# Kernel tuning notes

Measured on AMD Instinct MI355X. Metric: run time of the kernel, lower is better.

## Reference

```python
import jax, jax.numpy as jnp
import numpy as np

N_NODES = 100000
N_EDGES = 3200000
IN_DIM = 256
UNITS = 128


def setup_inputs() -> dict:
    key = jax.random.key(0)
    k1, k2, k3, k4, k5 = jax.random.split(key, 5)
    x = jax.random.normal(k1, (N_NODES, IN_DIM), dtype=jnp.float32)
    kernel = jax.random.normal(k2, (IN_DIM, UNITS), dtype=jnp.float32) * (1.0 / np.sqrt(IN_DIM))
    adj_rows = jax.random.randint(k3, (N_EDGES,), 0, N_NODES, dtype=jnp.int32)
    adj_cols = jax.random.randint(k4, (N_EDGES,), 0, N_NODES, dtype=jnp.int32)
    adj_vals = jax.random.uniform(k5, (N_EDGES,), dtype=jnp.float32)
    return {"x": x, "kernel": kernel, "adj_rows": adj_rows,
            "adj_cols": adj_cols, "adj_vals": adj_vals}


def reference(x, kernel, adj_rows, adj_cols, adj_vals):
    # Dense transform: [N, in_dim] @ [in_dim, units] -> [N, units]
    h = jnp.matmul(x, kernel)
    # SpMM: out[r] = sum_{edges e with row r} val[e] * h[col[e]]
    msgs = h[adj_cols] * adj_vals[:, None]            # [E, units] gather
    agg = jax.ops.segment_sum(msgs, adj_rows, num_segments=N_NODES)  # scatter-add
    # use_bias=False -> no bias add. Activation: relu.
    return jax.nn.relu(agg)
```

## Files before the change

kernel.cpp:

```cpp
#include <hip/hip_runtime.h>
#include <hip/hip_fp16.h>

#define UNITS 128
#define IN_DIM 256

#define BSHIFT 6
#define BROWS  64
#define NBMAX  1600
#define BCAP   2368
#define SEDGE  2816
#define BIN_SLICE 4096

#define GR   128
#define GKC  64
#define APAD 36
#define BPAD 72

typedef short bf16x8 __attribute__((ext_vector_type(8)));
typedef float f32x4  __attribute__((ext_vector_type(4)));
union FragU { uint4 u; bf16x8 f; };

__device__ inline unsigned short bf16_bits(float a) {
  unsigned u = __float_as_uint(a);
  return (unsigned short)((u + 0x7FFF + ((u >> 16) & 1)) >> 16);
}
__device__ inline unsigned pack_bf16x2(float a, float b) {
  return (unsigned)bf16_bits(a) | ((unsigned)bf16_bits(b) << 16);
}

__global__ __launch_bounds__(256) void wt_kernel(
    const float* __restrict__ W, unsigned short* __restrict__ WT) {
  const int i = blockIdx.x * 256 + threadIdx.x;
  const int k = i >> 7;
  const int n = i & 127;
  WT[n * IN_DIM + k] = bf16_bits(W[i]);
}

__device__ __forceinline__ void do_bin(
    int* sh_cnt, int bid,
    const int* __restrict__ rows, const int* __restrict__ cols,
    const float* __restrict__ vals, int* __restrict__ bcount,
    int2* __restrict__ binned, int n_edges, int nbuckets) {
  const int tid = threadIdx.x;
  const int e0 = bid * BIN_SLICE;
  const int e_end = min(e0 + BIN_SLICE, n_edges);

  for (int i = tid; i < nbuckets; i += 512) sh_cnt[i] = 0;
  __syncthreads();
#pragma unroll
  for (int p = 0; p < 2; ++p) {
    const int e = e0 + (tid + p * 512) * 4;
    if (e < e_end) {
      const int4 r4 = *(const int4*)(rows + e);
      atomicAdd(&sh_cnt[r4.x >> BSHIFT], 1);
      atomicAdd(&sh_cnt[r4.y >> BSHIFT], 1);
      atomicAdd(&sh_cnt[r4.z >> BSHIFT], 1);
      atomicAdd(&sh_cnt[r4.w >> BSHIFT], 1);
    }
  }
  __syncthreads();
  for (int i = tid; i < nbuckets; i += 512) {
    const int c = sh_cnt[i];
    sh_cnt[i] = c ? atomicAdd(&bcount[i], c) : 0;
  }
  __syncthreads();
#pragma unroll
  for (int p = 0; p < 2; ++p) {
    const int e = e0 + (tid + p * 512) * 4;
    if (e < e_end) {
      const int4   r4 = *(const int4*)(rows + e);
      const int4   c4 = *(const int4*)(cols + e);
      const float4 v4 = *(const float4*)(vals + e);
#pragma unroll
      for (int u = 0; u < 4; ++u) {
        const int rr = (&r4.x)[u];
        const int cc = (&c4.x)[u];
        const int b  = rr >> BSHIFT;
        const int pos = atomicAdd(&sh_cnt[b], 1);
        if (pos < BCAP)
          binned[(size_t)b * BCAP + pos] = make_int2(
              (int)(((unsigned)(rr & (BROWS - 1)) << 25) | ((unsigned)cc << 8)),
              __float_as_int((&v4.x)[u]));
      }
    }
  }
  __syncthreads();
}

__device__ __forceinline__ void do_gemm(
    char* smem, int bid,
    const float* __restrict__ x, const unsigned short* __restrict__ WT,
    __half* __restrict__ h, int n_nodes) {
  unsigned*       A_lds = (unsigned*)smem;
  unsigned short* B_lds = (unsigned short*)(smem + 18432);

  const int tid  = threadIdx.x;
  const int lane = tid & 63;
  const int wave = tid >> 6;
  const int row0 = bid * GR;
  const int m    = lane & 15;
  const int quad = lane >> 4;

  f32x4 acc[8];
#pragma unroll
  for (int i = 0; i < 8; ++i) acc[i] = (f32x4){0.f, 0.f, 0.f, 0.f};

  for (int k0 = 0; k0 < IN_DIM; k0 += GKC) {
#pragma unroll
    for (int p = 0; p < 4; ++p) {
      const int idx = tid + p * 512;
      const int rr  = idx >> 4;
      const int c4  = idx & 15;
      const int gr  = row0 + rr;
      float4 v = make_float4(0.f, 0.f, 0.f, 0.f);
      if (gr < n_nodes)
        v = *(const float4*)(x + (size_t)gr * IN_DIM + k0 + c4 * 4);
      unsigned* dst = &A_lds[rr * APAD + c4 * 2];
      dst[0] = pack_bf16x2(v.x, v.y);
      dst[1] = pack_bf16x2(v.z, v.w);
    }
#pragma unroll
    for (int p = 0; p < 2; ++p) {
      const int u = tid + p * 512;
      const int n = u >> 3;
      const int c = u & 7;
      const uint4 v = *(const uint4*)(WT + (size_t)n * IN_DIM + k0 + c * 8);
      *(uint4*)&B_lds[n * BPAD + c * 8] = v;
    }
    __syncthreads();

#pragma unroll
    for (int ks = 0; ks < 2; ++ks) {
      FragU a;
      a.u = *(const uint4*)&A_lds[(wave * 16 + m) * APAD + ks * 16 + quad * 4];
#pragma unroll
      for (int nt = 0; nt < 8; ++nt) {
        FragU b;
        b.u = *(const uint4*)&B_lds[(nt * 16 + m) * BPAD + ks * 32 + quad * 8];
        acc[nt] = __builtin_amdgcn_mfma_f32_16x16x32_bf16(a.f, b.f, acc[nt], 0, 0, 0);
      }
    }
    __syncthreads();
  }

  const int orow = row0 + wave * 16 + quad * 4;
#pragma unroll
  for (int nt = 0; nt < 8; ++nt) {
    const int col = nt * 16 + m;
#pragma unroll
    for (int i = 0; i < 4; ++i) {
      const int rr = orow + i;
      if (rr < n_nodes)
        h[(size_t)rr * UNITS + col] = __float2half(acc[nt][i]);
    }
  }
}

__global__ __launch_bounds__(512) void fused_gemm_bin_kernel(
    const float* __restrict__ x, const unsigned short* __restrict__ WT,
    __half* __restrict__ h,
    const int* __restrict__ rows, const int* __restrict__ cols,
    const float* __restrict__ vals, int* __restrict__ bcount,
    int2* __restrict__ binned, int n_nodes, int n_edges, int nbuckets) {
  __shared__ __align__(16) char smem[36864];
  const int bid = blockIdx.x;
  const bool bin_first = (bid & 1) == 0;

  if (bin_first)
    do_bin((int*)smem, bid, rows, cols, vals, bcount, binned, n_edges, nbuckets);
  do_gemm(smem, bid, x, WT, h, n_nodes);
  if (!bin_first)
    do_bin((int*)smem, bid, rows, cols, vals, bcount, binned, n_edges, nbuckets);
}

#define SA_TPB 256

__global__ __launch_bounds__(SA_TPB) void sortagg_kernel(
    const int* __restrict__ bcount, const int2* __restrict__ binned,
    const __half* __restrict__ h, float* __restrict__ out, int n_nodes) {
  __shared__ int2 sedge[SEDGE];
  __shared__ int  shist[BROWS];
  __shared__ int  sstart[BROWS + 1];
  __shared__ int  scur[BROWS];

  const int tid  = threadIdx.x;
  const int lane = tid & 63;
  const int wv   = tid >> 6;
  const int b    = blockIdx.x;
  const int row0 = b << BSHIFT;

  int cnt = bcount[b]; if (cnt > BCAP) cnt = BCAP;

  int2 my[10];
#pragma unroll
  for (int k = 0; k < 10; ++k) {
    const int j = tid + k * SA_TPB;
    my[k] = (j < cnt) ? binned[(size_t)b * BCAP + j] : make_int2(0, 0);
  }

#pragma unroll
  for (int k = 0; k < 11; ++k) {
    const int i = tid + k * SA_TPB;
    if (i < SEDGE) sedge[i] = make_int2(0, 0);
  }
  if (tid < BROWS) shist[tid] = 0;
  __syncthreads();

#pragma unroll
  for (int k = 0; k < 10; ++k) {
    const int j = tid + k * SA_TPB;
    if (j < cnt) atomicAdd(&shist[(unsigned)my[k].x >> 25], 1);
  }
  __syncthreads();

  if (wv == 0) {
    const int orig = shist[lane];
    const int pad  = (orig + 7) & ~7;
    int v = pad;
#pragma unroll
    for (int off = 1; off < 64; off <<= 1) {
      const int u = __shfl_up(v, off, 64);
      if (lane >= off) v += u;
    }
    sstart[lane] = v - pad;
    scur[lane]   = v - pad;
    if (lane == 63) sstart[64] = v;
  }
  __syncthreads();

#pragma unroll
  for (int k = 0; k < 10; ++k) {
    const int j = tid + k * SA_TPB;
    if (j < cnt) {
      const int rl  = (unsigned)my[k].x >> 25;
      const int pos = atomicAdd(&scur[rl], 1);
      sedge[pos] = make_int2(my[k].x & 0x01FFFF00, my[k].y);
    }
  }
  __syncthreads();

  const char* hb = (const char*)h + (lane << 2);
#pragma unroll 1
  for (int i = 0; i < 16; ++i) {
    const int rl  = wv * 16 + i;
    const int row = row0 + rl;
    if (row >= n_nodes) break;
    const int s = sstart[rl];
    const int e = sstart[rl + 1];
    float accx = 0.f, accy = 0.f;
    for (int j = s; j < e; j += 8) {
      float v[8]; float2 f[8];
#pragma unroll
      for (int u = 0; u < 8; ++u) {
        const int2 q = sedge[j + u];
        v[u] = __int_as_float(q.y);
        f[u] = __half22float2(*(const __half2*)(hb + (unsigned)q.x));
      }
#pragma unroll
      for (int u = 0; u < 8; ++u) {
        accx = fmaf(v[u], f[u].x, accx);
        accy = fmaf(v[u], f[u].y, accy);
      }
    }
    float2 o;
    o.x = accx > 0.f ? accx : 0.f;
    o.y = accy > 0.f ? accy : 0.f;
    ((float2*)(out + (size_t)row * UNITS))[lane] = o;
  }
}

extern "C" void kernel_launch(void* const* d_in, const int* in_sizes, int n_in,
                              void* d_out, int out_size, void* d_ws, size_t ws_size,
                              hipStream_t stream) {
  const float* x     = (const float*)d_in[0];
  const float* W     = (const float*)d_in[1];
  const int*   rows  = (const int*)d_in[2];
  const int*   cols  = (const int*)d_in[3];
  const float* vals  = (const float*)d_in[4];
  float*       out   = (float*)d_out;

  const int n_nodes = in_sizes[0] / IN_DIM;
  const int n_edges = in_sizes[2];
  const int nbuckets = (n_nodes + BROWS - 1) >> BSHIFT;

  char* ws = (char*)d_ws;
  size_t off = 0;
  auto alloc = [&](size_t bytes) {
    char* p = ws + off;
    off += (bytes + 511) & ~(size_t)511;
    return p;
  };
  __half*         h      = (__half*)alloc((size_t)n_nodes * UNITS * sizeof(__half));
  unsigned short* WT     = (unsigned short*)alloc((size_t)UNITS * IN_DIM * 2);
  int*            bcount = (int*)   alloc((size_t)nbuckets * sizeof(int));
  int2*           binned = (int2*)  alloc((size_t)nbuckets * BCAP * sizeof(int2));

  wt_kernel<<<(IN_DIM * UNITS) / 256, 256, 0, stream>>>(W, WT);
  hipMemsetAsync(bcount, 0, (size_t)nbuckets * sizeof(int), stream);

  const int nblocks = (n_nodes + GR - 1) / GR;
  fused_gemm_bin_kernel<<<nblocks, 512, 0, stream>>>(
      x, WT, h, rows, cols, vals, bcount, binned, n_nodes, n_edges, nbuckets);

  sortagg_kernel<<<nbuckets, SA_TPB, 0, stream>>>(bcount, binned, h, out, n_nodes);
}
```

Before: 379.0 us.

## Replace atomic global bucket binning with per-chunk counting sort and prefix offsets

```diff
diff --git a/kernel.cpp b/kernel.cpp
--- a/kernel.cpp
+++ b/kernel.cpp
@@ -4,12 +4,10 @@
 #define UNITS 128
 #define IN_DIM 256
 
-#define BSHIFT 6
-#define BROWS  64
-#define NBMAX  1600
-#define BCAP   2368
-#define SEDGE  2816
-#define BIN_SLICE 4096
+#define BROWS   98
+#define NBPAD   1024
+#define NCHUNK  64
+#define SEDGE   4272
 
 #define GR   128
 #define GKC  64
@@ -19,6 +17,10 @@
 typedef short bf16x8 __attribute__((ext_vector_type(8)));
 typedef float f32x4  __attribute__((ext_vector_type(4)));
 union FragU { uint4 u; bf16x8 f; };
+
+__device__ inline int bucket_of(int r) {
+  return (int)(unsigned)(((unsigned long long)(unsigned)r * 342393ull) >> 25);
+}
 
 __device__ inline unsigned short bf16_bits(float a) {
   unsigned u = __float_as_uint(a);
@@ -37,54 +39,66 @@
 }
 
 __device__ __forceinline__ void do_bin(
-    int* sh_cnt, int bid,
+    char* smem, int c,
     const int* __restrict__ rows, const int* __restrict__ cols,
-    const float* __restrict__ vals, int* __restrict__ bcount,
-    int2* __restrict__ binned, int n_edges, int nbuckets) {
+    const float* __restrict__ vals, int* __restrict__ cstart,
+    int2* __restrict__ binned, int n_edges, int nbuckets, int CS) {
+  int* hist = (int*)smem;
+  int* aux  = (int*)(smem + NBPAD * 4);
   const int tid = threadIdx.x;
-  const int e0 = bid * BIN_SLICE;
-  const int e_end = min(e0 + BIN_SLICE, n_edges);
-
-  for (int i = tid; i < nbuckets; i += 512) sh_cnt[i] = 0;
-  __syncthreads();
-#pragma unroll
-  for (int p = 0; p < 2; ++p) {
-    const int e = e0 + (tid + p * 512) * 4;
-    if (e < e_end) {
-      const int4 r4 = *(const int4*)(rows + e);
-      atomicAdd(&sh_cnt[r4.x >> BSHIFT], 1);
-      atomicAdd(&sh_cnt[r4.y >> BSHIFT], 1);
-      atomicAdd(&sh_cnt[r4.z >> BSHIFT], 1);
-      atomicAdd(&sh_cnt[r4.w >> BSHIFT], 1);
-    }
-  }
-  __syncthreads();
-  for (int i = tid; i < nbuckets; i += 512) {
-    const int c = sh_cnt[i];
-    sh_cnt[i] = c ? atomicAdd(&bcount[i], c) : 0;
-  }
-  __syncthreads();
-#pragma unroll
-  for (int p = 0; p < 2; ++p) {
-    const int e = e0 + (tid + p * 512) * 4;
-    if (e < e_end) {
-      const int4   r4 = *(const int4*)(rows + e);
-      const int4   c4 = *(const int4*)(cols + e);
-      const float4 v4 = *(const float4*)(vals + e);
-#pragma unroll
-      for (int u = 0; u < 4; ++u) {
-        const int rr = (&r4.x)[u];
-        const int cc = (&c4.x)[u];
-        const int b  = rr >> BSHIFT;
-        const int pos = atomicAdd(&sh_cnt[b], 1);
-        if (pos < BCAP)
-          binned[(size_t)b * BCAP + pos] = make_int2(
-              (int)(((unsigned)(rr & (BROWS - 1)) << 25) | ((unsigned)cc << 8)),
-              __float_as_int((&v4.x)[u]));
-      }
-    }
-  }
-  __syncthreads();
+  const int e0 = c * CS;
+  const int e_end = min(e0 + CS, n_edges);
+
+  for (int i = tid; i < NBPAD; i += 512) hist[i] = 0;
+  __syncthreads();
+
+  for (int e = e0 + tid * 4; e < e_end; e += 2048) {
+    const int4 r4 = *(const int4*)(rows + e);
+    atomicAdd(&hist[bucket_of(r4.x)], 1);
+    atomicAdd(&hist[bucket_of(r4.y)], 1);
+    atomicAdd(&hist[bucket_of(r4.z)], 1);
+    atomicAdd(&hist[bucket_of(r4.w)], 1);
+  }
+  __syncthreads();
+
+  const int a0 = hist[2 * tid];
+  const int a1 = hist[2 * tid + 1];
+  const int p  = a0 + a1;
+  aux[tid] = p;
+  __syncthreads();
+  for (int off = 1; off < 512; off <<= 1) {
+    int u = 0;
+    if (tid >= off) u = aux[tid - off];
+    __syncthreads();
+    if (tid >= off) aux[tid] += u;
+    __syncthreads();
+  }
+  const int excl = aux[tid] - p;
+  if (2 * tid <= nbuckets) {
+    hist[2 * tid] = excl;
+    cstart[c * NBPAD + 2 * tid] = excl;
+  }
+  if (2 * tid + 1 <= nbuckets) {
+    hist[2 * tid + 1] = excl + a0;
+    cstart[c * NBPAD + 2 * tid + 1] = excl + a0;
+  }
+  __syncthreads();
+
+  for (int e = e0 + tid * 4; e < e_end; e += 2048) {
+    const int4   r4 = *(const int4*)(rows + e);
+    const int4   c4 = *(const int4*)(cols + e);
+    const float4 v4 = *(const float4*)(vals + e);
+#pragma unroll
+    for (int u = 0; u < 4; ++u) {
+      const int r  = (&r4.x)[u];
+      const int b  = bucket_of(r);
+      const int rl = r - b * BROWS;
+      const int pos = atomicAdd(&hist[b], 1);
+      binned[(size_t)c * CS + pos] = make_int2(
+          (int)(((unsigned)rl << 25) | ((unsigned)(&c4.x)[u] << 8)),
+          __float_as_int((&v4.x)[u]));
+    }
+  }
 }
 
 __device__ __forceinline__ void do_gemm(
@@ -123,9 +137,9 @@
     for (int p = 0; p < 2; ++p) {
       const int u = tid + p * 512;
       const int n = u >> 3;
-      const int c = u & 7;
-      const uint4 v = *(const uint4*)(WT + (size_t)n * IN_DIM + k0 + c * 8);
-      *(uint4*)&B_lds[n * BPAD + c * 8] = v;
+      const int cc = u & 7;
+      const uint4 v = *(const uint4*)(WT + (size_t)n * IN_DIM + k0 + cc * 8);
+      *(uint4*)&B_lds[n * BPAD + cc * 8] = v;
     }
     __syncthreads();
 
@@ -160,89 +174,104 @@
     const float* __restrict__ x, const unsigned short* __restrict__ WT,
     __half* __restrict__ h,
     const int* __restrict__ rows, const int* __restrict__ cols,
-    const float* __restrict__ vals, int* __restrict__ bcount,
-    int2* __restrict__ binned, int n_nodes, int n_edges, int nbuckets) {
+    const float* __restrict__ vals, int* __restrict__ cstart,
+    int2* __restrict__ binned, int n_nodes, int n_edges, int nbuckets,
+    int CS) {
   __shared__ __align__(16) char smem[36864];
-  const int bid = blockIdx.x;
-  const bool bin_first = (bid & 1) == 0;
-
-  if (bin_first)
-    do_bin((int*)smem, bid, rows, cols, vals, bcount, binned, n_edges, nbuckets);
-  do_gemm(smem, bid, x, WT, h, n_nodes);
-  if (!bin_first)
-    do_bin((int*)smem, bid, rows, cols, vals, bcount, binned, n_edges, nbuckets);
-}
-
-#define SA_TPB 256
+  if (blockIdx.x < NCHUNK)
+    do_bin(smem, blockIdx.x, rows, cols, vals, cstart, binned,
+           n_edges, nbuckets, CS);
+  else
+    do_gemm(smem, blockIdx.x - NCHUNK, x, WT, h, n_nodes);
+}
+
+#define SA_TPB 512
 
 __global__ __launch_bounds__(SA_TPB) void sortagg_kernel(
-    const int* __restrict__ bcount, const int2* __restrict__ binned,
-    const __half* __restrict__ h, float* __restrict__ out, int n_nodes) {
+    const int* __restrict__ cstart, const int2* __restrict__ binned,
+    const __half* __restrict__ h, float* __restrict__ out,
+    int n_nodes, int nbuckets, int CS) {
   __shared__ int2 sedge[SEDGE];
   __shared__ int  shist[BROWS];
   __shared__ int  sstart[BROWS + 1];
   __shared__ int  scur[BROWS];
+  __shared__ int  sc[NCHUNK];
+  __shared__ int  scnt[NCHUNK];
 
   const int tid  = threadIdx.x;
   const int lane = tid & 63;
   const int wv   = tid >> 6;
   const int b    = blockIdx.x;
-  const int row0 = b << BSHIFT;
-
-  int cnt = bcount[b]; if (cnt > BCAP) cnt = BCAP;
-
-  int2 my[10];
-#pragma unroll
-  for (int k = 0; k < 10; ++k) {
-    const int j = tid + k * SA_TPB;
-    my[k] = (j < cnt) ? binned[(size_t)b * BCAP + j] : make_int2(0, 0);
-  }
-
-#pragma unroll
-  for (int k = 0; k < 11; ++k) {
-    const int i = tid + k * SA_TPB;
-    if (i < SEDGE) sedge[i] = make_int2(0, 0);
-  }
+  const int row0 = b * BROWS;
+
+  if (tid < NCHUNK) {
+    const int s  = cstart[tid * NBPAD + b];
+    const int e2 = cstart[tid * NBPAD + b + 1];
+    sc[tid]   = s;
+    scnt[tid] = e2 - s;
+  }
+  for (int i = tid; i < SEDGE; i += SA_TPB) sedge[i] = make_int2(0, 0);
   if (tid < BROWS) shist[tid] = 0;
   __syncthreads();
 
-#pragma unroll
-  for (int k = 0; k < 10; ++k) {
-    const int j = tid + k * SA_TPB;
-    if (j < cnt) atomicAdd(&shist[(unsigned)my[k].x >> 25], 1);
+#pragma unroll 1
+  for (int k = 0; k < 8; ++k) {
+    const int c   = wv * 8 + k;
+    const int cnt = scnt[c];
+    const size_t base = (size_t)c * CS + sc[c];
+    for (int j = lane; j < cnt; j += 64)
+      atomicAdd(&shist[(unsigned)binned[base + j].x >> 25], 1);
   }
   __syncthreads();
 
   if (wv == 0) {
-    const int orig = shist[lane];
-    const int pad  = (orig + 7) & ~7;
-    int v = pad;
+    const int v0 = shist[lane];
+    const int p0 = (v0 + 7) & ~7;
+    int s = p0;
 #pragma unroll
     for (int off = 1; off < 64; off <<= 1) {
-      const int u = __shfl_up(v, off, 64);
-      if (lane >= off) v += u;
-    }
-    sstart[lane] = v - pad;
-    scur[lane]   = v - pad;
-    if (lane == 63) sstart[64] = v;
-  }
-  __syncthreads();
-
-#pragma unroll
-  for (int k = 0; k < 10; ++k) {
-    const int j = tid + k * SA_TPB;
-    if (j < cnt) {
-      const int rl  = (unsigned)my[k].x >> 25;
+      const int u = __shfl_up(s, off, 64);
+      if (lane >= off) s += u;
+    }
+    sstart[lane] = s - p0;
+    scur[lane]   = s - p0;
+    const int t0 = __shfl(s, 63, 64);
+    const int idx = 64 + lane;
+    const int v1 = (idx < BROWS) ? shist[idx] : 0;
+    const int p1 = (idx < BROWS) ? ((v1 + 7) & ~7) : 0;
+    int s1 = p1;
+#pragma unroll
+    for (int off = 1; off < 64; off <<= 1) {
+      const int u = __shfl_up(s1, off, 64);
+      if (lane >= off) s1 += u;
+    }
+    if (idx < BROWS) {
+      sstart[idx] = t0 + s1 - p1;
+      scur[idx]   = t0 + s1 - p1;
+    }
+    if (lane == 63) sstart[BROWS] = t0 + s1;
+  }
+  __syncthreads();
+
+#pragma unroll 1
+  for (int k = 0; k < 8; ++k) {
+    const int c   = wv * 8 + k;
+    const int cnt = scnt[c];
+    const size_t base = (size_t)c * CS + sc[c];
+    for (int j = lane; j < cnt; j += 64) {
+      const int2 q = binned[base + j];
+      const int rl = (unsigned)q.x >> 25;
       const int pos = atomicAdd(&scur[rl], 1);
-      sedge[pos] = make_int2(my[k].x & 0x01FFFF00, my[k].y);
+      sedge[pos] = make_int2(q.x & 0x01FFFF00, q.y);
     }
   }
   __syncthreads();
 
   const char* hb = (const char*)h + (lane << 2);
 #pragma unroll 1
-  for (int i = 0; i < 16; ++i) {
-    const int rl  = wv * 16 + i;
+  for (int i = 0; i < 13; ++i) {
+    const int rl = wv + i * 8;
+    if (rl >= BROWS) break;
     const int row = row0 + rl;
     if (row >= n_nodes) break;
     const int s = sstart[rl];
@@ -281,7 +310,8 @@
 
   const int n_nodes = in_sizes[0] / IN_DIM;
   const int n_edges = in_sizes[2];
-  const int nbuckets = (n_nodes + BROWS - 1) >> BSHIFT;
+  const int nbuckets = (n_nodes + BROWS - 1) / BROWS;
+  const int CS = ((n_edges + NCHUNK - 1) / NCHUNK + 3) & ~3;
 
   char* ws = (char*)d_ws;
   size_t off = 0;
@@ -292,15 +322,15 @@
   };
   __half*         h      = (__half*)alloc((size_t)n_nodes * UNITS * sizeof(__half));
   unsigned short* WT     = (unsigned short*)alloc((size_t)UNITS * IN_DIM * 2);
-  int*            bcount = (int*)   alloc((size_t)nbuckets * sizeof(int));
-  int2*           binned = (int2*)  alloc((size_t)nbuckets * BCAP * sizeof(int2));
+  int*            cstart = (int*)   alloc((size_t)NCHUNK * NBPAD * sizeof(int));
+  int2*           binned = (int2*)  alloc((size_t)NCHUNK * CS * sizeof(int2));
 
   wt_kernel<<<(IN_DIM * UNITS) / 256, 256, 0, stream>>>(W, WT);
-  hipMemsetAsync(bcount, 0, (size_t)nbuckets * sizeof(int), stream);
-
-  const int nblocks = (n_nodes + GR - 1) / GR;
-  fused_gemm_bin_kernel<<<nblocks, 512, 0, stream>>>(
-      x, WT, h, rows, cols, vals, bcount, binned, n_nodes, n_edges, nbuckets);
-
-  sortagg_kernel<<<nbuckets, SA_TPB, 0, stream>>>(bcount, binned, h, out, n_nodes);
-}
+
+  const int ntiles = (n_nodes + GR - 1) / GR;
+  fused_gemm_bin_kernel<<<NCHUNK + ntiles, 512, 0, stream>>>(
+      x, WT, h, rows, cols, vals, cstart, binned, n_nodes, n_edges, nbuckets, CS);
+
+  sortagg_kernel<<<nbuckets, SA_TPB, 0, stream>>>(
+      cstart, binned, h, out, n_nodes, nbuckets, CS);
+}
```

Result: slower. 401.0 us (+5.8%).
